# Kernel tuning notes

Measured on AMD Instinct MI355X. Metric: run time of the kernel, lower is better.

Reference implementation:

```python
import jax, jax.numpy as jnp
import numpy as np

DEGREE = 3        # self.degree = 3 in MGNN
K = 3             # Chebyshev/polynomial order of the GCN
BANDWIDTH = 512.0 # Gaussian kernel bandwidth (~2*d so adj spans (0,1])
B, N, D_IN = 2, 4096, 256
D_OUT = 64        # 2*D_OUT == 128 == linear output dim


def _bspline(t, degree):
    """Cox-de Boor recursive B-spline basis N_{0,degree}(t), elementwise,
    uniform knots on [0,1]. t: [B,N,N] adjacency values."""
    knots = np.linspace(0.0, 1.0, degree + 2)  # static python floats
    basis = [jnp.where((t >= knots[i]) & (t < knots[i + 1]), 1.0, 0.0).astype(t.dtype)
             for i in range(degree + 1)]
    for k in range(1, degree + 1):
        basis = [
            (t - knots[i]) / (knots[i + k] - knots[i]) * basis[i]
            + (knots[i + k + 1] - t) / (knots[i + k + 1] - knots[i + 1]) * basis[i + 1]
            for i in range(degree + 1 - k)
        ]
    return basis[0]


def _wavelet(t, degree):
    # spline wavelet: difference of dilated/shifted B-splines
    return _bspline(2.0 * t, degree) - _bspline(2.0 * t - 1.0, degree)


def _graph_construction(x, bandwidth):
    # Gaussian-kernel dense adjacency per batch element: [B,N,N], values in (0,1]
    sq = jnp.sum(x * x, axis=-1)                                   # [B,N]
    d2 = sq[:, :, None] + sq[:, None, :] - 2.0 * jnp.einsum('bnd,bmd->bnm', x, x)
    d2 = jnp.maximum(d2, 0.0)
    return jnp.exp(-d2 / bandwidth)


def _gcn(x, kernel, Wk):
    # out = sum_k (kernel^k x) W_k ; Wk: [K, D_IN, D_OUT]
    h = x
    out = jnp.einsum('bnd,do->bno', h, Wk[0])
    for k in range(1, Wk.shape[0]):
        h = jnp.einsum('bnm,bmd->bnd', kernel, h)
        out = out + jnp.einsum('bnd,do->bno', h, Wk[k])
    return out


def setup_inputs() -> dict:
    key = jax.random.key(0)
    k0, k1, k2, k3 = jax.random.split(key, 4)
    x = jax.random.normal(k0, (B, N, D_IN), dtype=jnp.float32)
    Wk = jax.random.normal(k1, (K, D_IN, D_OUT), dtype=jnp.float32) * 0.05
    W_lin = jax.random.normal(k2, (D_IN, 2 * D_OUT), dtype=jnp.float32) * 0.05
    b_lin = jnp.zeros((2 * D_OUT,), dtype=jnp.float32)
    return {"x": x, "Wk": Wk, "W_lin": W_lin, "b_lin": b_lin}


def reference(x, Wk, W_lin, b_lin):
    adj = _graph_construction(x, BANDWIDTH)       # [B,N,N]
    b_kernel = _bspline(adj, DEGREE)              # [B,N,N]
    w_kernel = _wavelet(adj, DEGREE)              # [B,N,N]
    gcn1 = _gcn(x, b_kernel, Wk)                  # [B,N,D_OUT]
    gcn2 = _gcn(x, w_kernel, Wk)                  # [B,N,D_OUT]
    akgcn = jnp.concatenate([gcn1, gcn2], axis=-1)        # [B,N,2*D_OUT]
    akgcn = jax.nn.relu(akgcn + x @ W_lin + b_lin)        # residual + relu
    return akgcn.reshape(akgcn.shape[0], -1)              # flatten last two dims
```

## Files before the change

kernel.cpp:

```cpp
#include <hip/hip_runtime.h>
#include <hip/hip_bf16.h>

typedef __hip_bfloat16 bf16;
typedef float v4f __attribute__((ext_vector_type(4)));
typedef short v8s __attribute__((ext_vector_type(8)));

typedef const __attribute__((address_space(1))) void gvoid;
typedef __attribute__((address_space(3))) void lvoid;

__device__ __forceinline__ void async16(const void* g, void* l) {
  __builtin_amdgcn_global_load_lds((gvoid*)g, (lvoid*)l, 16, 0, 0);
}

__device__ __forceinline__ float b3(float u) {
  u = fminf(fmaxf(u, 0.f), 4.f);
  float t1 = fmaxf(u - 1.f, 0.f);
  float t2 = fmaxf(u - 2.f, 0.f);
  float t3 = fmaxf(u - 3.f, 0.f);
  float c0 = u * u * u;
  float c1 = t1 * t1 * t1;
  float c2 = t2 * t2 * t2;
  float c3 = t3 * t3 * t3;
  return (c0 - 4.f * c1 + 6.f * c2 - 4.f * c3) * (1.f / 6.f);
}

template <int NI, int BK>
__device__ __forceinline__ void mfma_loop(const bf16* __restrict__ A,
                                          const bf16* __restrict__ B, int lda,
                                          int ldb, int kLen, bf16* As, bf16* Bs,
                                          v4f acc[4][NI]) {
  const int tid = threadIdx.x;
  const int wave = tid >> 6;
  const int lane = tid & 63;
  const int quad = lane >> 4;
  const int r16 = lane & 15;
  const int wm = (wave >> 1) * 64;
  const int wn = (wave & 1) * (NI * 16);
  constexpr int CPR = BK / 8;
  constexpr int AQ = 128 * CPR / 256;
  constexpr int BQ = NI * 32 * CPR / 256;
  char* AsC = (char*)As;
  char* BsC = (char*)Bs;
  for (int kk = 0; kk < kLen; kk += BK) {
#pragma unroll
    for (int q = 0; q < AQ; ++q) {
      const int ch = tid + 256 * q;
      const int r = ch / CPR, c = (ch % CPR) * 8;
      async16(A + (size_t)r * lda + kk + c, AsC + q * 4096 + wave * 1024);
    }
#pragma unroll
    for (int q = 0; q < BQ; ++q) {
      const int ch = tid + 256 * q;
      const int r = ch / CPR, c = (ch % CPR) * 8;
      async16(B + (size_t)r * ldb + kk + c, BsC + q * 4096 + wave * 1024);
    }
    __syncthreads();
#pragma unroll
    for (int ks = 0; ks < BK / 32; ++ks) {
      v8s af[4], bfr[NI];
#pragma unroll
      for (int mi = 0; mi < 4; ++mi)
        af[mi] =
            *(const v8s*)(As + (wm + mi * 16 + r16) * BK + ks * 32 + quad * 8);
#pragma unroll
      for (int ni = 0; ni < NI; ++ni)
        bfr[ni] =
            *(const v8s*)(Bs + (wn + ni * 16 + r16) * BK + ks * 32 + quad * 8);
#pragma unroll
      for (int mi = 0; mi < 4; ++mi)
#pragma unroll
        for (int ni = 0; ni < NI; ++ni)
          acc[mi][ni] = __builtin_amdgcn_mfma_f32_16x16x32_bf16(
              af[mi], bfr[ni], acc[mi][ni], 0, 0, 0);
    }
    __syncthreads();
  }
}

__global__ void prep(const float* __restrict__ x, bf16* __restrict__ U,
                     float* __restrict__ sq) {
  const int n = blockIdx.x, b = blockIdx.y, t = threadIdx.x;
  const size_t row = (size_t)b * 4096 + n;
  float v = x[row * 256 + t];
  U[row * 1280 + t] = __float2bfloat16(v);
  float s = v * v;
#pragma unroll
  for (int o = 32; o > 0; o >>= 1) s += __shfl_down(s, o, 64);
  __shared__ float ls[4];
  if ((t & 63) == 0) ls[t >> 6] = s;
  __syncthreads();
  if (t == 0) sq[row] = ls[0] + ls[1] + ls[2] + ls[3];
}

__global__ void transk(const float* __restrict__ src, bf16* __restrict__ dst) {
  __shared__ float tile[64][65];
  const int z = blockIdx.z;
  const float* s = src + (size_t)z * 4096 * 256;
  bf16* d = dst + (size_t)z * 256 * 4096;
  const int n0 = blockIdx.x * 64, d0 = blockIdx.y * 64;
  const int tx = threadIdx.x & 31, ty = threadIdx.x >> 5;
#pragma unroll
  for (int i = 0; i < 8; ++i) {
    const int r = ty + i * 8;
    const float2 v = *(const float2*)(s + (size_t)(n0 + r) * 256 + d0 + tx * 2);
    tile[r][tx * 2] = v.x;
    tile[r][tx * 2 + 1] = v.y;
  }
  __syncthreads();
#pragma unroll
  for (int i = 0; i < 8; ++i) {
    const int c = ty + i * 8;
    __hip_bfloat162 p;
    p.x = __float2bfloat16(tile[tx * 2][c]);
    p.y = __float2bfloat16(tile[tx * 2 + 1][c]);
    *(__hip_bfloat162*)(d + (size_t)(d0 + c) * 4096 + n0 + tx * 2) = p;
  }
}

__global__ void wbig(const float* __restrict__ Wk, const float* __restrict__ Wl,
                     bf16* __restrict__ WbT) {
  int idx = blockIdx.x * 256 + threadIdx.x;
  if (idx >= 128 * 1280) return;
  int j = idx / 1280, k = idx % 1280;
  int o = j & 63;
  float v = 0.f;
  if (k < 256)
    v = Wk[k * 64 + o] + Wl[k * 128 + j];
  else if (k < 512)
    v = (j < 64) ? Wk[16384 + (k - 256) * 64 + o] : 0.f;
  else if (k < 768)
    v = (j < 64) ? Wk[32768 + (k - 512) * 64 + o] : 0.f;
  else if (k < 1024)
    v = (j >= 64) ? Wk[16384 + (k - 768) * 64 + o] : 0.f;
  else
    v = (j >= 64) ? Wk[32768 + (k - 1024) * 64 + o] : 0.f;
  WbT[idx] = __float2bfloat16(v);
}

__global__ __launch_bounds__(256, 2) void gemm_s(const bf16* __restrict__ U,
                                                 const float* __restrict__ sq,
                                                 bf16* __restrict__ kmat) {
  __shared__ __align__(16) bf16 As[128 * 64];
  __shared__ __align__(16) bf16 Bs[128 * 64];
  __shared__ unsigned lut[4096];
  const int tid = threadIdx.x;
  for (int i = tid; i < 4096; i += 256) {
    float t = (i + 0.5f) * (1.f / 4096.f);
    float bv = b3(4.f * t);
    float wv = b3(8.f * t) - b3(8.f * t - 4.f);
    __hip_bfloat162 p;
    p.x = __float2bfloat16(bv);
    p.y = __float2bfloat16(wv);
    lut[i] = *(unsigned*)&p;
  }
  const int z = blockIdx.z;
  const bf16* A = U + (size_t)z * 4096 * 1280 + (size_t)blockIdx.x * 128 * 1280;
  const bf16* B = U + (size_t)z * 4096 * 1280 + (size_t)blockIdx.y * 128 * 1280;
  v4f acc[4][4];
#pragma unroll
  for (int a = 0; a < 4; ++a)
#pragma unroll
    for (int b2 = 0; b2 < 4; ++b2) acc[a][b2] = (v4f){0.f, 0.f, 0.f, 0.f};
  mfma_loop<4, 64>(A, B, 1280, 1280, 256, As, Bs, acc);
  const int wave = tid >> 6, lane = tid & 63;
  const int quad = lane >> 4, r16 = lane & 15;
  const int wm = (wave >> 1) * 64, wn = (wave & 1) * 64;
  const float* sqr = sq + (size_t)z * 4096;
  unsigned short* bk = (unsigned short*)(kmat + (size_t)(z * 2) * 4096 * 4096);
  unsigned short* wk = bk + (size_t)4096 * 4096;
  const int i0 = blockIdx.x * 128 + wm + quad * 4;
  const int j0 = blockIdx.y * 128 + wn + r16;
  float sqj[4];
#pragma unroll
  for (int ni = 0; ni < 4; ++ni) sqj[ni] = sqr[j0 + ni * 16];
  const float c = -1.4426950408889634f / 512.f;
#pragma unroll
  for (int mi = 0; mi < 4; ++mi) {
#pragma unroll
    for (int r = 0; r < 4; ++r) {
      const int i = i0 + mi * 16 + r;
      const float si = sqr[i];
#pragma unroll
      for (int ni = 0; ni < 4; ++ni) {
        const int j = j0 + ni * 16;
        float s = acc[mi][ni][r];
        float d2 = fmaxf(si + sqj[ni] - 2.f * s, 0.f);
        float t = __builtin_amdgcn_exp2f(d2 * c);
        int idx = (int)fminf(t * 4096.f, 4095.f);
        unsigned pv = lut[idx];
        size_t off = (size_t)i * 4096 + j;
        bk[off] = (unsigned short)(pv & 0xffff);
        wk[off] = (unsigned short)(pv >> 16);
      }
    }
  }
}

__global__ __launch_bounds__(256, 4) void gemm_h(const bf16* __restrict__ kmat,
                                                 const bf16* __restrict__ BtBase,
                                                 float* __restrict__ hpart,
                                                 int btShift) {
  __shared__ __align__(16) bf16 As[128 * 64];
  __shared__ __align__(16) bf16 Bs[128 * 64];
  const int bz = blockIdx.z;
  const int z = bz >> 2, split = bz & 3;
  const int kk0 = split * 1024;
  const bf16* A =
      kmat + (size_t)z * 4096 * 4096 + (size_t)blockIdx.x * 128 * 4096 + kk0;
  const bf16* B = BtBase + (size_t)(z >> btShift) * 256 * 4096 +
                  (size_t)blockIdx.y * 128 * 4096 + kk0;
  v4f acc[4][4];
#pragma unroll
  for (int a = 0; a < 4; ++a)
#pragma unroll
    for (int b2 = 0; b2 < 4; ++b2) acc[a][b2] = (v4f){0.f, 0.f, 0.f, 0.f};
  mfma_loop<4, 64>(A, B, 4096, 4096, 1024, As, Bs, acc);
  const int tid = threadIdx.x, wave = tid >> 6, lane = tid & 63;
  const int quad = lane >> 4, r16 = lane & 15;
  const int wm = (wave >> 1) * 64, wn = (wave & 1) * 64;
  float* H = hpart + ((size_t)split * 4 + z) * 4096 * 256;
  const int i0 = blockIdx.x * 128 + wm + quad * 4;
  const int j0 = blockIdx.y * 128 + wn + r16;
#pragma unroll
  for (int mi = 0; mi < 4; ++mi)
#pragma unroll
    for (int r = 0; r < 4; ++r) {
      const int i = i0 + mi * 16 + r;
#pragma unroll
      for (int ni = 0; ni < 4; ++ni)
        H[(size_t)i * 256 + j0 + ni * 16] = acc[mi][ni][r];
    }
}

__global__ void reduceT(const float* __restrict__ hpart, bf16* __restrict__ U,
                        bf16* __restrict__ hT, int uoffBase) {
  __shared__ float tile[64][65];
  const int z = blockIdx.z;
  const int b = z >> 1, kern = z & 1;
  const int uoff = uoffBase + kern * 512;
  const int n0 = blockIdx.x * 64, d0 = blockIdx.y * 64;
  const int tx = threadIdx.x & 31, ty = threadIdx.x >> 5;
  const size_t sstride = (size_t)4 * 4096 * 256;
  const float* s0 = hpart + (size_t)z * 4096 * 256;
#pragma unroll
  for (int i = 0; i < 8; ++i) {
    const int r = ty + i * 8;
    const size_t off = (size_t)(n0 + r) * 256 + d0 + tx * 2;
    float vx = 0.f, vy = 0.f;
#pragma unroll
    for (int k = 0; k < 4; ++k) {
      const float2 a = *(const float2*)(s0 + k * sstride + off);
      vx += a.x;
      vy += a.y;
    }
    tile[r][tx * 2] = vx;
    tile[r][tx * 2 + 1] = vy;
    __hip_bfloat162 p;
    p.x = __float2bfloat16(vx);
    p.y = __float2bfloat16(vy);
    *(__hip_bfloat162*)(U + (size_t)(b * 4096 + n0 + r) * 1280 + uoff + d0 +
                        tx * 2) = p;
  }
  if (hT) {
    __syncthreads();
#pragma unroll
    for (int i = 0; i < 8; ++i) {
      const int c = ty + i * 8;
      __hip_bfloat162 p;
      p.x = __float2bfloat16(tile[tx * 2][c]);
      p.y = __float2bfloat16(tile[tx * 2 + 1][c]);
      *(__hip_bfloat162*)(hT + (size_t)z * 256 * 4096 + (size_t)(d0 + c) * 4096 +
                          n0 + tx * 2) = p;
    }
  }
}

__global__ __launch_bounds__(256, 4) void gemm_proj(
    const bf16* __restrict__ U, const bf16* __restrict__ WbT,
    const float* __restrict__ blin, float* __restrict__ out) {
  __shared__ __align__(16) bf16 As[128 * 64];
  __shared__ __align__(16) bf16 Bs[64 * 64];
  const bf16* A = U + (size_t)blockIdx.x * 128 * 1280;
  const bf16* B = WbT + (size_t)blockIdx.y * 64 * 1280;
  v4f acc[4][2];
#pragma unroll
  for (int a = 0; a < 4; ++a)
#pragma unroll
    for (int b2 = 0; b2 < 2; ++b2) acc[a][b2] = (v4f){0.f, 0.f, 0.f, 0.f};
  mfma_loop<2, 64>(A, B, 1280, 1280, 1280, As, Bs, acc);
  const int tid = threadIdx.x, wave = tid >> 6, lane = tid & 63;
  const int quad = lane >> 4, r16 = lane & 15;
  const int wm = (wave >> 1) * 64, wn = (wave & 1) * 32;
  const int i0 = blockIdx.x * 128 + wm + quad * 4;
  const int j0 = blockIdx.y * 64 + wn + r16;
#pragma unroll
  for (int mi = 0; mi < 4; ++mi)
#pragma unroll
    for (int r = 0; r < 4; ++r) {
      const int i = i0 + mi * 16 + r;
#pragma unroll
      for (int ni = 0; ni < 2; ++ni) {
        const int j = j0 + ni * 16;
        out[(size_t)i * 128 + j] = fmaxf(acc[mi][ni][r] + blin[j], 0.f);
      }
    }
}

extern "C" void kernel_launch(void* const* d_in, const int* in_sizes, int n_in,
                              void* d_out, int out_size, void* d_ws,
                              size_t ws_size, hipStream_t stream) {
  const float* x = (const float*)d_in[0];
  const float* Wk = (const float*)d_in[1];
  const float* Wlin = (const float*)d_in[2];
  const float* blin = (const float*)d_in[3];
  float* out = (float*)d_out;
  char* w = (char*)d_ws;
  bf16* kmat = (bf16*)(w);
  float* hpart = (float*)(w + 134217728);
  bf16* h1T = (bf16*)(w + 201326592);
  bf16* xhT = (bf16*)(w + 209715200);
  bf16* U = (bf16*)(w + 213909504);
  bf16* WbT = (bf16*)(w + 234881024);
  float* sqv = (float*)(w + 235208704);

  prep<<<dim3(4096, 2), 256, 0, stream>>>(x, U, sqv);
  transk<<<dim3(64, 4, 2), 256, 0, stream>>>(x, xhT);
  wbig<<<dim3(640), 256, 0, stream>>>(Wk, Wlin, WbT);
  gemm_s<<<dim3(32, 32, 2), 256, 0, stream>>>(U, sqv, kmat);
  gemm_h<<<dim3(32, 2, 16), 256, 0, stream>>>(kmat, xhT, hpart, 1);
  reduceT<<<dim3(64, 4, 4), 256, 0, stream>>>(hpart, U, h1T, 256);
  gemm_h<<<dim3(32, 2, 16), 256, 0, stream>>>(kmat, h1T, hpart, 0);
  reduceT<<<dim3(64, 4, 4), 256, 0, stream>>>(hpart, U, nullptr, 512);
  gemm_proj<<<dim3(64, 2), 256, 0, stream>>>(U, WbT, blin, out);
}
```

Measured before the change: 256.8 us.

## Pair adjacent lanes to write 32-bit kernel stores and shrink LUT for occupancy

The epilogue of the S-GEMM now exchanges LUT results between neighbouring lanes so each lane writes packed 32-bit words of two adjacent bf16 values instead of 16-bit scalar stores, which halves store instructions to the large kernel matrices. The LUT is halved to 2048 entries and launch bounds raised to 4 waves per SIMD, cutting LDS use to allow more resident blocks. Row norms are also preloaded into registers. The coarser LUT slightly changes quantization of the spline values, and the higher occupancy target may force register spills.

```diff
diff --git a/kernel.cpp b/kernel.cpp
--- a/kernel.cpp
+++ b/kernel.cpp
@@ -137,15 +137,15 @@
   WbT[idx] = __float2bfloat16(v);
 }
 
-__global__ __launch_bounds__(256, 2) void gemm_s(const bf16* __restrict__ U,
+__global__ __launch_bounds__(256, 4) void gemm_s(const bf16* __restrict__ U,
                                                  const float* __restrict__ sq,
                                                  bf16* __restrict__ kmat) {
   __shared__ __align__(16) bf16 As[128 * 64];
   __shared__ __align__(16) bf16 Bs[128 * 64];
-  __shared__ unsigned lut[4096];
+  __shared__ unsigned lut[2048];
   const int tid = threadIdx.x;
-  for (int i = tid; i < 4096; i += 256) {
-    float t = (i + 0.5f) * (1.f / 4096.f);
+  for (int i = tid; i < 2048; i += 256) {
+    float t = (i + 0.5f) * (1.f / 2048.f);
     float bv = b3(4.f * t);
     float wv = b3(8.f * t) - b3(8.f * t - 4.f);
     __hip_bfloat162 p;
@@ -170,27 +170,45 @@
   unsigned short* wk = bk + (size_t)4096 * 4096;
   const int i0 = blockIdx.x * 128 + wm + quad * 4;
   const int j0 = blockIdx.y * 128 + wn + r16;
+  const int par = lane & 1;
+  const int jc = j0 - par;
   float sqj[4];
 #pragma unroll
   for (int ni = 0; ni < 4; ++ni) sqj[ni] = sqr[j0 + ni * 16];
   const float c = -1.4426950408889634f / 512.f;
+  float si[16];
+#pragma unroll
+  for (int mi = 0; mi < 4; ++mi)
+#pragma unroll
+    for (int r = 0; r < 4; ++r) si[mi * 4 + r] = sqr[i0 + mi * 16 + r];
 #pragma unroll
   for (int mi = 0; mi < 4; ++mi) {
 #pragma unroll
-    for (int r = 0; r < 4; ++r) {
-      const int i = i0 + mi * 16 + r;
-      const float si = sqr[i];
-#pragma unroll
-      for (int ni = 0; ni < 4; ++ni) {
-        const int j = j0 + ni * 16;
+    for (int ni = 0; ni < 4; ++ni) {
+      unsigned pv[4];
+#pragma unroll
+      for (int r = 0; r < 4; ++r) {
         float s = acc[mi][ni][r];
-        float d2 = fmaxf(si + sqj[ni] - 2.f * s, 0.f);
+        float d2 = fmaxf(si[mi * 4 + r] + sqj[ni] - 2.f * s, 0.f);
         float t = __builtin_amdgcn_exp2f(d2 * c);
-        int idx = (int)fminf(t * 4096.f, 4095.f);
-        unsigned pv = lut[idx];
-        size_t off = (size_t)i * 4096 + j;
-        bk[off] = (unsigned short)(pv & 0xffff);
-        wk[off] = (unsigned short)(pv >> 16);
+        int idx = (int)fminf(t * 2048.f, 2047.f);
+        pv[r] = lut[idx];
+      }
+      unsigned ov[4];
+#pragma unroll
+      for (int r = 0; r < 4; ++r) ov[r] = __shfl_xor((int)pv[r], 1, 64);
+#pragma unroll
+      for (int rr = 0; rr < 2; ++rr) {
+        const int r = par * 2 + rr;
+        const unsigned a = pv[r], b2 = ov[r];
+        const unsigned lo = par ? b2 : a;
+        const unsigned hi = par ? a : b2;
+        const unsigned bkd = (lo & 0xffffu) | (hi << 16);
+        const unsigned wkd = (lo >> 16) | (hi & 0xffff0000u);
+        const int i = i0 + mi * 16 + r;
+        const size_t off = (size_t)i * 4096 + jc + ni * 16;
+        *(unsigned*)(bk + off) = bkd;
+        *(unsigned*)(wk + off) = wkd;
       }
     }
   }
```

New measurement: 254.3 us. No clear change (-1.0%).
